# Kernel tuning notes

Measured on AMD Instinct MI355X. Metric: run time of the kernel, lower is better.

Reference implementation:

```python
import jax, jax.numpy as jnp
import numpy as np

N, E, D, H, FF = 50000, 1600000, 128, 8, 512
DK = D // H
EPS = 1e-5


def _layernorm(x, g, b):
    mu = jnp.mean(x, axis=-1, keepdims=True)
    var = jnp.mean((x - mu) ** 2, axis=-1, keepdims=True)
    return (x - mu) * jax.lax.rsqrt(var + EPS) * g + b


def setup_inputs() -> dict:
    key = jax.random.key(0)
    ks = jax.random.split(key, 10)
    s = 0.05
    return {
        "h": jax.random.normal(ks[0], (N, D), jnp.float32),
        "src": jax.random.randint(ks[1], (E,), 0, N, jnp.int32),
        "dst": jax.random.randint(ks[2], (E,), 0, N, jnp.int32),
        "Wq": jax.random.normal(ks[3], (D, D), jnp.float32) * s,
        "Wk": jax.random.normal(ks[4], (D, D), jnp.float32) * s,
        "Wv": jax.random.normal(ks[5], (D, D), jnp.float32) * s,
        "Wo": jax.random.normal(ks[6], (D, D), jnp.float32) * s,
        "ln1_g": jnp.ones((D,), jnp.float32),
        "ln1_b": jnp.zeros((D,), jnp.float32),
        "ln2_g": jnp.ones((D,), jnp.float32),
        "ln2_b": jnp.zeros((D,), jnp.float32),
        "W1": jax.random.normal(ks[7], (D, FF), jnp.float32) * s,
        "b1": jnp.zeros((FF,), jnp.float32),
        "W2": jax.random.normal(ks[8], (FF, D), jnp.float32) * s,
        "b2": jnp.zeros((D,), jnp.float32),
    }


def reference(h, src, dst, Wq, Wk, Wv, Wo, ln1_g, ln1_b, ln2_g, ln2_b, W1, b1, W2, b2):
    # QKV projections (bias-free, as in the torch module)
    q = (h @ Wq).reshape(N, H, DK)
    k = (h @ Wk).reshape(N, H, DK)
    v = (h @ Wv).reshape(N, H, DK)

    # masked_mm: per-edge, per-head score  e[m,h] = q[dst[m]] . k[src[m]]
    e = jnp.einsum("ehd,ehd->eh", q[dst], k[src]) / np.sqrt(DK)

    # sparse_softmax: segment softmax over incoming edges of each dst node
    m = jax.ops.segment_max(e, dst, num_segments=N)  # [N, H]
    ex = jnp.exp(e - m[dst])
    denom = jax.ops.segment_sum(ex, dst, num_segments=N)  # [N, H]
    alpha = ex / denom[dst]  # [E, H]

    # vec_spmm: a[n] = sum_{edges m with dst[m]==n} alpha[m] * v[src[m]]
    a = jax.ops.segment_sum(alpha[:, :, None] * v[src], dst, num_segments=N)
    a = a.reshape(N, D)

    o = a @ Wo
    h1 = _layernorm(h + o, ln1_g, ln1_b)
    ffn = jax.nn.relu(h1 @ W1 + b1) @ W2 + b2
    h2 = _layernorm(h1 + ffn, ln2_g, ln2_b)
    return h2
```

## Files before the change

kernel.cpp:

```cpp
#include <hip/hip_runtime.h>
#include <hip/hip_bf16.h>
#include <math.h>

#define D   128
#define FFD 512
#define NPART 8
#define BINB 1024
#define BCAP 768
#define NPROD 32
#define NSUB 32
#define RCAP 320

typedef __attribute__((ext_vector_type(8))) short bf16x8;
typedef __attribute__((ext_vector_type(4))) float f32x4;
typedef __attribute__((ext_vector_type(2))) float f32x2;

static inline size_t align256(size_t x){ return (x + 255) & ~(size_t)255; }

__device__ __forceinline__ float bf2f(unsigned short u){
    union { unsigned int i; float f; } x; x.i = ((unsigned int)u) << 16; return x.f;
}
__device__ __forceinline__ unsigned short f2bf(float f){
    return __builtin_bit_cast(unsigned short, __float2bfloat16(f));
}
__device__ __forceinline__ unsigned char f2fp8(float f){
    return (unsigned char)(__builtin_amdgcn_cvt_pk_fp8_f32(f, f, 0, false) & 0xff);
}

#define DPP_ADD(x, ctrl) do { \
    int yi_ = __builtin_amdgcn_update_dpp(0, __builtin_bit_cast(int, x), ctrl, 0xf, 0xf, true); \
    x += __builtin_bit_cast(float, yi_); } while(0)

__global__ __launch_bounds__(256) void k_bin3(const int* __restrict__ src,
                                              const int* __restrict__ dst, int E, int N,
                                              unsigned long long* __restrict__ pairs,
                                              int* __restrict__ lens,
                                              unsigned long long* __restrict__ spill,
                                              int* __restrict__ qspill){
    __shared__ int lcur[8];
    int tid = threadIdx.x;
    if (tid < 8) lcur[tid] = 0;
    __syncthreads();
    int slice = (N + 7) >> 3;
    int T = gridDim.x * 256;
    unsigned long long* myreg = pairs + (size_t)blockIdx.x * 8 * BCAP;
    for (int i = blockIdx.x*256 + tid; i < E; i += T){
        int d = __builtin_nontemporal_load(&dst[i]);
        int s = __builtin_nontemporal_load(&src[i]);
        int b = min(d / slice, 7);
        unsigned long long pr = ((unsigned long long)(unsigned)d << 32) | (unsigned)s;
        int slot = atomicAdd(&lcur[b], 1);
        if (slot < BCAP) myreg[(size_t)b*BCAP + slot] = pr;
        else { int p = atomicAdd(qspill, 1); spill[p] = pr; }
    }
    __syncthreads();
    if (tid < 8) lens[blockIdx.x*8 + tid] = min(lcur[tid], BCAP);
}

__global__ __launch_bounds__(256) void k_rebin(const unsigned long long* __restrict__ pairs,
                                               const int* __restrict__ lens,
                                               unsigned* __restrict__ pairs2,
                                               int* __restrict__ rlens,
                                               unsigned long long* __restrict__ spill,
                                               int* __restrict__ qspill, int N){
    __shared__ int lcur[NSUB];
    int part = blockIdx.x & 7, ip = blockIdx.x >> 3;
    int tid = threadIdx.x;
    if (tid < NSUB) lcur[tid] = 0;
    __syncthreads();
    int slice = (N + 7) >> 3;
    unsigned subslice = (unsigned)(slice + NSUB - 1) / NSUB;
    int lo_part = part * slice;
    unsigned* outbase = pairs2 + (size_t)(part*NPROD + ip) * NSUB * RCAP;
    for (int seg = ip*(BINB/NPROD); seg < (ip+1)*(BINB/NPROD); ++seg){
        int len = lens[seg*8 + part];
        const unsigned long long* pp = pairs + ((size_t)seg*8 + part)*BCAP;
        for (int i = tid; i < len; i += 256){
            unsigned long long pr = pp[i];
            int d = (int)(pr >> 32);
            unsigned dl = (unsigned)(d - lo_part);
            unsigned sb = dl / subslice;
            int slot = atomicAdd(&lcur[sb], 1);
            if (slot < RCAP)
                outbase[(size_t)sb*RCAP + slot] = ((dl - sb*subslice) << 24) | (unsigned)pr & 0xFFFFFFu;
            else { int p = atomicAdd(qspill, 1); spill[p] = pr; }
        }
    }
    __syncthreads();
    if (tid < NSUB) rlens[(part*NPROD + ip)*NSUB + tid] = min(lcur[tid], RCAP);
}

__global__ __launch_bounds__(256) void k_count4(const unsigned* __restrict__ pairs2,
                                                const int* __restrict__ rlens,
                                                const unsigned long long* __restrict__ spill,
                                                const int* __restrict__ qspill,
                                                int* __restrict__ cnt, int N){
    __shared__ int hist[256];
    int part = blockIdx.x & 7, s = blockIdx.x >> 3;
    int slice = (N + 7) >> 3;
    int subslice = (slice + NSUB - 1) / NSUB;
    int lo_part = part*slice;
    int lo = lo_part + s*subslice;
    int part_end = min(lo_part + slice, N);
    int n_sub = max(0, min(subslice, part_end - lo));
    for (int i = threadIdx.x; i < 256; i += 256) hist[i] = 0;
    __syncthreads();
    for (int ip = 0; ip < NPROD; ++ip){
        int r = (part*NPROD + ip)*NSUB + s;
        int len = rlens[r];
        const unsigned* pp = pairs2 + (size_t)r*RCAP;
        for (int i = threadIdx.x; i < len; i += 256)
            atomicAdd(&hist[pp[i] >> 24], 1);
    }
    int ns = *qspill;
    for (int i = threadIdx.x; i < ns; i += 256){
        int r = (int)(spill[i] >> 32) - lo;
        if (r >= 0 && r < n_sub) atomicAdd(&hist[r], 1);
    }
    __syncthreads();
    for (int i = threadIdx.x; i < n_sub; i += 256) cnt[lo + i] = hist[i];
}

__global__ __launch_bounds__(256) void k_scatter4(const unsigned* __restrict__ pairs2,
                                                  const int* __restrict__ rlens,
                                                  const unsigned long long* __restrict__ spill,
                                                  const int* __restrict__ qspill,
                                                  const int* __restrict__ off,
                                                  int* __restrict__ csr_src, int N){
    __shared__ int curl[256];
    int part = blockIdx.x & 7, s = blockIdx.x >> 3;
    int slice = (N + 7) >> 3;
    int subslice = (slice + NSUB - 1) / NSUB;
    int lo_part = part*slice;
    int lo = lo_part + s*subslice;
    int part_end = min(lo_part + slice, N);
    int n_sub = max(0, min(subslice, part_end - lo));
    for (int i = threadIdx.x; i < n_sub; i += 256) curl[i] = off[lo + i];
    __syncthreads();
    for (int ip = 0; ip < NPROD; ++ip){
        int r = (part*NPROD + ip)*NSUB + s;
        int len = rlens[r];
        const unsigned* pp = pairs2 + (size_t)r*RCAP;
        for (int i = threadIdx.x; i < len; i += 256){
            unsigned e = pp[i];
            int pos = atomicAdd(&curl[e >> 24], 1);
            csr_src[pos] = (int)(e & 0xFFFFFFu);
        }
    }
    int ns = *qspill;
    for (int i = threadIdx.x; i < ns; i += 256){
        unsigned long long pr = spill[i];
        int r = (int)(pr >> 32) - lo;
        if (r >= 0 && r < n_sub){
            int pos = atomicAdd(&curl[r], 1);
            csr_src[pos] = (int)(unsigned)pr;
        }
    }
}

__global__ __launch_bounds__(256) void k_bsum(const int* __restrict__ cnt, int N,
                                              int* __restrict__ bsum){
    int id = blockIdx.x*256 + threadIdx.x;
    int v = (id < N) ? cnt[id] : 0;
    #pragma unroll
    for (int o = 1; o < 64; o <<= 1) v += __shfl_xor(v, o);
    __shared__ int w4[4];
    if ((threadIdx.x & 63) == 0) w4[threadIdx.x >> 6] = v;
    __syncthreads();
    if (threadIdx.x == 0) bsum[blockIdx.x] = w4[0] + w4[1] + w4[2] + w4[3];
}

__global__ __launch_bounds__(1024) void k_scanb(const int* __restrict__ bsum, int NB,
                                                int* __restrict__ ebase,
                                                int* __restrict__ off, int N){
    __shared__ int sh[1024];
    int tid = threadIdx.x;
    int v = (tid < NB) ? bsum[tid] : 0;
    sh[tid] = v; __syncthreads();
    for (int o = 1; o < 1024; o <<= 1){
        int t = (tid >= o) ? sh[tid-o] : 0;
        __syncthreads();
        sh[tid] += t;
        __syncthreads();
    }
    if (tid < NB) ebase[tid] = sh[tid] - v;
    if (tid == NB-1) off[N] = sh[tid];
}

__global__ __launch_bounds__(256) void k_off(const int* __restrict__ cnt, int N,
                                             const int* __restrict__ ebase,
                                             int* __restrict__ off){
    __shared__ int sh[256];
    int tid = threadIdx.x;
    int id = blockIdx.x*256 + tid;
    int v = (id < N) ? cnt[id] : 0;
    sh[tid] = v; __syncthreads();
    for (int o = 1; o < 256; o <<= 1){
        int t = (tid >= o) ? sh[tid-o] : 0;
        __syncthreads();
        sh[tid] += t;
        __syncthreads();
    }
    int excl = sh[tid] - v;
    int base = ebase[blockIdx.x];
    if (id < N) off[id] = base + excl;
}

__global__ __launch_bounds__(256) void k_cast(const float* __restrict__ x,
                                              __hip_bfloat16* __restrict__ y, int n4){
    int i = blockIdx.x*blockDim.x + threadIdx.x;
    if (i >= n4) return;
    float4 f = ((const float4*)x)[i];
    ushort4 u;
    u.x = f2bf(f.x); u.y = f2bf(f.y);
    u.z = f2bf(f.z); u.w = f2bf(f.w);
    ((ushort4*)y)[i] = u;
}

__global__ __launch_bounds__(256) void k_prep_all(
    const float* __restrict__ Wq, const float* __restrict__ Wk,
    const float* __restrict__ Wv, const float* __restrict__ Wo,
    const float* __restrict__ W1, const float* __restrict__ W2,
    __hip_bfloat16* __restrict__ Wqkvt, __hip_bfloat16* __restrict__ Wot,
    __hip_bfloat16* __restrict__ W1t,   __hip_bfloat16* __restrict__ W2t){
    const float* W; __hip_bfloat16* Wt; int K, Nc;
    int y = blockIdx.y;
    switch (y){
        case 0: W = Wq; Wt = Wqkvt; K = 128; Nc = 128; break;
        case 1: W = Wk; Wt = Wqkvt; K = 128; Nc = 128; break;
        case 2: W = Wv; Wt = Wqkvt; K = 128; Nc = 128; break;
        case 3: W = Wo; Wt = Wot;   K = 128; Nc = 128; break;
        case 4: W = W1; Wt = W1t;   K = 128; Nc = 512; break;
        default: W = W2; Wt = W2t;  K = 512; Nc = 128; break;
    }
    int total = K*Nc;
    for (int id = blockIdx.x*256 + threadIdx.x; id < total; id += 256*gridDim.x){
        int n = id / K, kk = id % K;
        size_t drow;
        if (y == 1)      drow = 128 + 8*(n>>2) + (n&3);
        else if (y == 2) drow = 128 + 8*(n>>2) + 4 + (n&3);
        else             drow = n;
        Wt[drow*K + kk] = __float2bfloat16(W[(size_t)kk*Nc + n]);
    }
}

#define BM 128
#define BN 128
#define BK 64

__device__ __forceinline__ bool tile_coords(int M, int &r0, int &c0){
    int ncols = gridDim.x;
    int f = blockIdx.y * ncols + blockIdx.x;
    int xcd = f & 7, s = f >> 3;
    int c = s % ncols, rl = s / ncols;
    int r = rl*8 + xcd;
    r0 = r*BM; c0 = c*BN;
    return r0 < M;
}

__device__ __forceinline__ void stage_tile(const __hip_bfloat16* __restrict__ src,
                                           int row_base, int row_limit, int ldK, int k0,
                                           __hip_bfloat16* lds){
    int tid = threadIdx.x;
    int wave = tid >> 6;
    #pragma unroll
    for (int i = 0; i < 4; ++i){
        int c = i*256 + tid;
        int r = c >> 3, s = c & 7;
        int sg = s ^ (r & 7);
        int gr = row_base + r; if (gr >= row_limit) gr = row_limit - 1;
        const __hip_bfloat16* gp = src + (size_t)gr*ldK + k0 + sg*8;
        char* lp = (char*)lds + (i*256 + wave*64)*16;
        __builtin_amdgcn_global_load_lds((const __attribute__((address_space(1))) void*)gp,
                                         (__attribute__((address_space(3))) void*)lp,
                                         16, 0, 0);
    }
}

__device__ __forceinline__ bf16x8 frag(const __hip_bfloat16* buf, int R, int kk, int ls){
    int sl = (kk*4 + ls) ^ (R & 7);
    return *(const bf16x8*)((const char*)buf + R*128 + sl*16);
}

__global__ __launch_bounds__(256) void k_gemm_qkv(
    const __hip_bfloat16* __restrict__ A,
    const __hip_bfloat16* __restrict__ Bt,
    int M,
    __hip_bfloat16* __restrict__ qb, unsigned char* __restrict__ kvq){
    __shared__ __hip_bfloat16 As[BM*BK];
    __shared__ __hip_bfloat16 Bs[BN*BK];
    int r0, c0;
    if (!tile_coords(M, r0, c0)) return;
    int tid = threadIdx.x;
    int lane = tid & 63, wave = tid >> 6;
    int wr = wave >> 1, wc = wave & 1;
    int lr = lane & 15, ls = lane >> 4;

    f32x4 acc[4][4];
    #pragma unroll
    for (int m = 0; m < 4; m++)
        #pragma unroll
        for (int n = 0; n < 4; n++) acc[m][n] = (f32x4){0.f,0.f,0.f,0.f};

    for (int k0 = 0; k0 < 128; k0 += BK){
        stage_tile(A,  r0, M,   128, k0, As);
        stage_tile(Bt, c0, 384, 128, k0, Bs);
        __syncthreads();
        #pragma unroll
        for (int kk = 0; kk < 2; ++kk){
            bf16x8 af[4], bfg[4];
            #pragma unroll
            for (int m = 0; m < 4; m++) af[m]  = frag(As, wr*64 + m*16 + lr, kk, ls);
            #pragma unroll
            for (int n = 0; n < 4; n++) bfg[n] = frag(Bs, wc*64 + n*16 + lr, kk, ls);
            #pragma unroll
            for (int m = 0; m < 4; m++)
                #pragma unroll
                for (int n = 0; n < 4; n++)
                    acc[m][n] = __builtin_amdgcn_mfma_f32_16x16x32_bf16(af[m], bfg[n], acc[m][n], 0, 0, 0);
        }
        __syncthreads();
    }

    int region = c0 >> 7;
    #pragma unroll
    for (int n = 0; n < 4; n++){
        int c16 = wc*64 + n*16 + lr;
        #pragma unroll
        for (int m = 0; m < 4; m++){
            #pragma unroll
            for (int j = 0; j < 4; j++){
                int row = r0 + wr*64 + m*16 + ls*4 + j;
                if (row >= M) continue;
                float v = acc[m][n][j];
                if (region == 0)
                    ((unsigned short*)qb)[(size_t)row*128 + c16] = f2bf(v);
                else
                    kvq[(size_t)row*256 + (region-1)*128 + c16] = f2fp8(v);
            }
        }
    }
}

__global__ __launch_bounds__(256) void k_tail(
    const __hip_bfloat16* __restrict__ ab, const float* __restrict__ h,
    const __hip_bfloat16* __restrict__ Wot,
    const float* __restrict__ ln1g, const float* __restrict__ ln1b,
    const __hip_bfloat16* __restrict__ W1t, const float* __restrict__ b1,
    const __hip_bfloat16* __restrict__ W2t, const float* __restrict__ b2,
    const float* __restrict__ ln2g, const float* __restrict__ ln2b,
    float* __restrict__ out, int M){
    __shared__ __hip_bfloat16 As[BM*BK];
    __shared__ __hip_bfloat16 Bs[BM*BK];
    __shared__ __hip_bfloat16 h1s[2][BM*BK];
    __shared__ __hip_bfloat16 t1s[2][BM*BK];
    __shared__ float red[2][BM][2];
    int f = blockIdx.x;
    int r0 = ((f >> 3)*8 + (f & 7)) * BM;
    if (r0 >= M) return;
    int tid = threadIdx.x;
    int lane = tid & 63, wave = tid >> 6;
    int wr = wave >> 1, wc = wave & 1;
    int lr = lane & 15, ls = lane >> 4;

    f32x4 acc[4][4];
    #pragma unroll
    for (int m = 0; m < 4; m++)
        #pragma unroll
        for (int n = 0; n < 4; n++) acc[m][n] = (f32x4){0.f,0.f,0.f,0.f};

    for (int k0 = 0; k0 < 128; k0 += BK){
        stage_tile(ab,  r0, M,   128, k0, As);
        stage_tile(Wot, 0,  128, 128, k0, Bs);
        __syncthreads();
        #pragma unroll
        for (int kk = 0; kk < 2; ++kk){
            bf16x8 af[4], bfg[4];
            #pragma unroll
            for (int m = 0; m < 4; m++) af[m]  = frag(As, wr*64 + m*16 + lr, kk, ls);
            #pragma unroll
            for (int n = 0; n < 4; n++) bfg[n] = frag(Bs, wc*64 + n*16 + lr, kk, ls);
            #pragma unroll
            for (int m = 0; m < 4; m++)
                #pragma unroll
                for (int n = 0; n < 4; n++)
                    acc[m][n] = __builtin_amdgcn_mfma_f32_16x16x32_bf16(af[m], bfg[n], acc[m][n], 0, 0, 0);
        }
        __syncthreads();
    }

    #pragma unroll
    for (int m = 0; m < 4; m++){
        #pragma unroll
        for (int j = 0; j < 4; j++){
            int rowl = wr*64 + m*16 + ls*4 + j;
            int row = r0 + rowl;
            float s = 0.f, q = 0.f;
            #pragma unroll
            for (int n = 0; n < 4; n++){
                int col = wc*64 + n*16 + lr;
                float rv = (row < M) ? h[(size_t)row*128 + col] : 0.f;
                float v = acc[m][n][j] + rv;
                acc[m][n][j] = v;
                s += v; q += v*v;
            }
            #pragma unroll
            for (int o = 1; o < 16; o <<= 1){
                s += __shfl_xor(s, o);
                q += __shfl_xor(q, o);
            }
            if (lr == 0){
                red[0][rowl][wc] = s;
                red[1][rowl][wc] = q;
            }
        }
    }
    __syncthreads();
    #pragma unroll
    for (int m = 0; m < 4; m++){
        #pragma unroll
        for (int j = 0; j < 4; j++){
            int rowl = wr*64 + m*16 + ls*4 + j;
            float mu  = (red[0][rowl][0] + red[0][rowl][1]) * (1.f/128.f);
            float eq  = (red[1][rowl][0] + red[1][rowl][1]) * (1.f/128.f);
            float var = fmaxf(eq - mu*mu, 0.f);
            float inv = rsqrtf(var + 1e-5f);
            #pragma unroll
            for (int n = 0; n < 4; n++){
                int col = wc*64 + n*16 + lr;
                float o = (acc[m][n][j] - mu)*inv*ln1g[col] + ln1b[col];
                int half = col >> 6, c6 = col & 63;
                int slot = (c6 >> 3) ^ (rowl & 7), elem = c6 & 7;
                ((unsigned short*)h1s[half])[rowl*64 + slot*8 + elem] = f2bf(o);
            }
        }
    }
    __syncthreads();

    f32x4 yacc[4][4];
    #pragma unroll
    for (int m = 0; m < 4; m++)
        #pragma unroll
        for (int n = 0; n < 4; n++) yacc[m][n] = (f32x4){0.f,0.f,0.f,0.f};

    for (int c = 0; c < 4; ++c){
        f32x4 tacc[4][4];
        #pragma unroll
        for (int m = 0; m < 4; m++)
            #pragma unroll
            for (int n = 0; n < 4; n++) tacc[m][n] = (f32x4){0.f,0.f,0.f,0.f};
        for (int step = 0; step < 2; ++step){
            stage_tile(W1t, c*128, 512, 128, step*64, Bs);
            __syncthreads();
            #pragma unroll
            for (int kk = 0; kk < 2; ++kk){
                bf16x8 af[4], bfg[4];
                #pragma unroll
                for (int m = 0; m < 4; m++) af[m]  = frag(h1s[step], wr*64 + m*16 + lr, kk, ls);
                #pragma unroll
                for (int n = 0; n < 4; n++) bfg[n] = frag(Bs, wc*64 + n*16 + lr, kk, ls);
                #pragma unroll
                for (int m = 0; m < 4; m++)
                    #pragma unroll
                    for (int n = 0; n < 4; n++)
                        tacc[m][n] = __builtin_amdgcn_mfma_f32_16x16x32_bf16(af[m], bfg[n], tacc[m][n], 0, 0, 0);
            }
            __syncthreads();
        }
        #pragma unroll
        for (int m = 0; m < 4; m++){
            #pragma unroll
            for (int j = 0; j < 4; j++){
                int rowl = wr*64 + m*16 + ls*4 + j;
                #pragma unroll
                for (int n = 0; n < 4; n++){
                    int col = wc*64 + n*16 + lr;
                    float v = fmaxf(tacc[m][n][j] + b1[c*128 + col], 0.f);
                    int half = col >> 6, c6 = col & 63;
                    int slot = (c6 >> 3) ^ (rowl & 7), elem = c6 & 7;
                    ((unsigned short*)t1s[half])[rowl*64 + slot*8 + elem] = f2bf(v);
                }
            }
        }
        __syncthreads();
        for (int step = 0; step < 2; ++step){
            stage_tile(W2t, 0, 128, 512, c*128 + step*64, Bs);
            __syncthreads();
            #pragma unroll
            for (int kk = 0; kk < 2; ++kk){
                bf16x8 af[4], bfg[4];
                #pragma unroll
                for (int m = 0; m < 4; m++) af[m]  = frag(t1s[step], wr*64 + m*16 + lr, kk, ls);
                #pragma unroll
                for (int n = 0; n < 4; n++) bfg[n] = frag(Bs, wc*64 + n*16 + lr, kk, ls);
                #pragma unroll
                for (int m = 0; m < 4; m++)
                    #pragma unroll
                    for (int n = 0; n < 4; n++)
                        yacc[m][n] = __builtin_amdgcn_mfma_f32_16x16x32_bf16(af[m], bfg[n], yacc[m][n], 0, 0, 0);
            }
            __syncthreads();
        }
    }

    #pragma unroll
    for (int m = 0; m < 4; m++){
        #pragma unroll
        for (int j = 0; j < 4; j++){
            int rowl = wr*64 + m*16 + ls*4 + j;
            float s = 0.f, q = 0.f;
            #pragma unroll
            for (int n = 0; n < 4; n++){
                int col = wc*64 + n*16 + lr;
                int half = col >> 6, c6 = col & 63;
                int slot = (c6 >> 3) ^ (rowl & 7), elem = c6 & 7;
                float h1v = bf2f(((const unsigned short*)h1s[half])[rowl*64 + slot*8 + elem]);
                float v = yacc[m][n][j] + b2[col] + h1v;
                yacc[m][n][j] = v;
                s += v; q += v*v;
            }
            #pragma unroll
            for (int o = 1; o < 16; o <<= 1){
                s += __shfl_xor(s, o);
                q += __shfl_xor(q, o);
            }
            if (lr == 0){
                red[0][rowl][wc] = s;
                red[1][rowl][wc] = q;
            }
        }
    }
    __syncthreads();
    #pragma unroll
    for (int m = 0; m < 4; m++){
        #pragma unroll
        for (int j = 0; j < 4; j++){
            int rowl = wr*64 + m*16 + ls*4 + j;
            int row = r0 + rowl;
            if (row >= M) continue;
            float mu  = (red[0][rowl][0] + red[0][rowl][1]) * (1.f/128.f);
            float eq  = (red[1][rowl][0] + red[1][rowl][1]) * (1.f/128.f);
            float var = fmaxf(eq - mu*mu, 0.f);
            float inv = rsqrtf(var + 1e-5f);
            #pragma unroll
            for (int n = 0; n < 4; n++){
                int col = wc*64 + n*16 + lr;
                out[(size_t)row*128 + col] = (yacc[m][n][j] - mu)*inv*ln2g[col] + ln2b[col];
            }
        }
    }
}

#define PAIR(jj, dd, b0, b1, b2, b3) { \
    int s0_ = __builtin_amdgcn_readlane(myidx, (jj)); \
    int s1_ = __builtin_amdgcn_readlane(myidx, (jj)+1); \
    int sv_ = half ? s1_ : s0_; \
    uint2 u_ = kv[(size_t)(unsigned)sv_*32 + l32]; \
    f32x2 k01 = __builtin_amdgcn_cvt_pk_f32_fp8((int)u_.x, false); \
    f32x2 k23 = __builtin_amdgcn_cvt_pk_f32_fp8((int)u_.x, true); \
    f32x2 v01 = __builtin_amdgcn_cvt_pk_f32_fp8((int)u_.y, false); \
    f32x2 v23 = __builtin_amdgcn_cvt_pk_f32_fp8((int)u_.y, true); \
    float p_ = q0*k01[0] + q1*k01[1] + q2*k23[0] + q3*k23[1]; \
    DPP_ADD(p_, 0xB1); DPP_ADD(p_, 0x4E); \
    float w_ = __builtin_amdgcn_exp2f(p_); \
    dd += w_; \
    b0 = fmaf(w_, v01[0], b0); b1 = fmaf(w_, v01[1], b1); \
    b2 = fmaf(w_, v23[0], b2); b3 = fmaf(w_, v23[1], b3); }

#define PAIRV(jj, dd, b0, b1, b2, b3) { \
    int s0_ = __builtin_amdgcn_readlane(myidx, (jj)); \
    int s1_ = __builtin_amdgcn_readlane(myidx, min((jj)+1, 63)); \
    int sv_ = half ? s1_ : s0_; \
    uint2 u_ = kv[(size_t)(unsigned)sv_*32 + l32]; \
    f32x2 k01 = __builtin_amdgcn_cvt_pk_f32_fp8((int)u_.x, false); \
    f32x2 k23 = __builtin_amdgcn_cvt_pk_f32_fp8((int)u_.x, true); \
    f32x2 v01 = __builtin_amdgcn_cvt_pk_f32_fp8((int)u_.y, false); \
    f32x2 v23 = __builtin_amdgcn_cvt_pk_f32_fp8((int)u_.y, true); \
    float p_ = q0*k01[0] + q1*k01[1] + q2*k23[0] + q3*k23[1]; \
    DPP_ADD(p_, 0xB1); DPP_ADD(p_, 0x4E); \
    float w_ = __builtin_amdgcn_exp2f(p_); \
    if ((jj) + half >= cnt) w_ = 0.f; \
    dd += w_; \
    b0 = fmaf(w_, v01[0], b0); b1 = fmaf(w_, v01[1], b1); \
    b2 = fmaf(w_, v23[0], b2); b3 = fmaf(w_, v23[1], b3); }

__global__ __launch_bounds__(256) void k_attn(const __hip_bfloat16* __restrict__ qb,
                                              const uint2* __restrict__ kv,
                                              const int* __restrict__ off,
                                              const int* __restrict__ csr_src,
                                              __hip_bfloat16* __restrict__ a, int N){
    int wid = (blockIdx.x*blockDim.x + threadIdx.x) >> 6;
    int lane = threadIdx.x & 63;
    if (wid >= N) return;
    int half = lane >> 5, l32 = lane & 31;
    ushort4 qu = ((const ushort4*)(qb + (size_t)wid*128))[l32];
    const float SC = 0.25f * 1.44269504f;
    float q0 = bf2f(qu.x)*SC, q1 = bf2f(qu.y)*SC, q2 = bf2f(qu.z)*SC, q3 = bf2f(qu.w)*SC;
    int beg = off[wid], end = off[wid+1];
    float dA=0, a0A=0, a1A=0, a2A=0, a3A=0;
    float dB=0, a0B=0, a1B=0, a2B=0, a3B=0;
    for (int e0 = beg; e0 < end; e0 += 64){
        int myidx = (e0 + lane < end) ? csr_src[e0 + lane] : 0;
        int cnt = min(64, end - e0);
        int j = 0;
        for (; j + 3 < cnt; j += 4){
            PAIR(j,   dA, a0A, a1A, a2A, a3A);
            PAIR(j+2, dB, a0B, a1B, a2B, a3B);
        }
        for (; j < cnt; j += 2){
            PAIRV(j, dA, a0A, a1A, a2A, a3A);
        }
    }
    float d  = dA + dB;
    float a0 = a0A + a0B, a1 = a1A + a1B, a2 = a2A + a2B, a3 = a3A + a3B;
    d  += __shfl_xor(d, 32);
    a0 += __shfl_xor(a0, 32);
    a1 += __shfl_xor(a1, 32);
    a2 += __shfl_xor(a2, 32);
    a3 += __shfl_xor(a3, 32);
    if (half == 0){
        float r = (d > 0.f) ? 1.f/d : 0.f;
        ushort4 o;
        o.x = f2bf(a0*r); o.y = f2bf(a1*r); o.z = f2bf(a2*r); o.w = f2bf(a3*r);
        ((ushort4*)(a + (size_t)wid*128))[l32] = o;
    }
}

extern "C" void kernel_launch(void* const* d_in, const int* in_sizes, int n_in,
                              void* d_out, int out_size, void* d_ws, size_t ws_size,
                              hipStream_t stream){
    const float* h    = (const float*)d_in[0];
    const int*   src  = (const int*)  d_in[1];
    const int*   dst  = (const int*)  d_in[2];
    const float* Wq   = (const float*)d_in[3];
    const float* Wk   = (const float*)d_in[4];
    const float* Wv   = (const float*)d_in[5];
    const float* Wo   = (const float*)d_in[6];
    const float* ln1g = (const float*)d_in[7];
    const float* ln1b = (const float*)d_in[8];
    const float* ln2g = (const float*)d_in[9];
    const float* ln2b = (const float*)d_in[10];
    const float* W1   = (const float*)d_in[11];
    const float* b1   = (const float*)d_in[12];
    const float* W2   = (const float*)d_in[13];
    const float* b2   = (const float*)d_in[14];
    float* out = (float*)d_out;

    const int N = in_sizes[0] / D;
    const int E = in_sizes[1];

    char* ws = (char*)d_ws;
    size_t o = 0;
    const size_t row_bf = align256((size_t)N * D * sizeof(__hip_bfloat16));
    const size_t kv_q   = align256((size_t)N * 256);

    __hip_bfloat16* qb  = (__hip_bfloat16*)(ws + o); o += row_bf;
    unsigned char* kvq  = (unsigned char*)(ws + o); o += kv_q;
    __hip_bfloat16* ab  = (__hip_bfloat16*)(ws + o); o += row_bf;
    __hip_bfloat16* hb  = (__hip_bfloat16*)(ws + o); o += row_bf;
    __hip_bfloat16* Wqkvt = (__hip_bfloat16*)(ws + o); o += align256(384*128*2);
    __hip_bfloat16* W1t   = (__hip_bfloat16*)(ws + o); o += align256(512*128*2);
    __hip_bfloat16* W2t   = (__hip_bfloat16*)(ws + o); o += align256(128*512*2);
    __hip_bfloat16* Wot   = (__hip_bfloat16*)(ws + o); o += align256(128*128*2);
    int* cnt   = (int*)(ws + o); o += align256((size_t)N*4);
    int* offp  = (int*)(ws + o); o += align256((size_t)(N+1)*4);
    int* bsum  = (int*)(ws + o); o += align256(1024*4);
    int* ebase = (int*)(ws + o); o += align256(1024*4);
    int* lens  = (int*)(ws + o); o += align256((size_t)BINB*8*4);
    int* rlens = (int*)(ws + o); o += align256((size_t)NPART*NPROD*NSUB*4);
    int* qspill= (int*)(ws + o); o += align256(256);
    int* csr   = (int*)(ws + o); o += align256((size_t)E*4);
    unsigned long long* pairs = (unsigned long long*)(ws + o);
    o += align256((size_t)BINB * 8 * BCAP * 8);
    unsigned* pairs2 = (unsigned*)(ws + o);
    o += align256((size_t)NPART * NPROD * NSUB * RCAP * 4);
    unsigned long long* spill = (unsigned long long*)(ws + o);
    o += align256((size_t)E * 8);

    const int NB = (N + 255)/256;

    (void)hipMemsetAsync(qspill, 0, 256, stream);
    k_bin3<<<BINB, 256, 0, stream>>>(src, dst, E, N, pairs, lens, spill, qspill);

    k_cast<<<(N*D/4 + 255)/256, 256, 0, stream>>>(h, hb, N*D/4);
    k_prep_all<<<dim3(64, 6), 256, 0, stream>>>(Wq, Wk, Wv, Wo, W1, W2,
                                                Wqkvt, Wot, W1t, W2t);

    k_rebin<<<NPART*NPROD, 256, 0, stream>>>(pairs, lens, pairs2, rlens, spill, qspill, N);
    k_count4<<<NPART*NSUB, 256, 0, stream>>>(pairs2, rlens, spill, qspill, cnt, N);
    k_bsum <<<NB, 256, 0, stream>>>(cnt, N, bsum);
    k_scanb<<<1, 1024, 0, stream>>>(bsum, NB, ebase, offp, N);
    k_off  <<<NB, 256, 0, stream>>>(cnt, N, ebase, offp);
    k_scatter4<<<NPART*NSUB, 256, 0, stream>>>(pairs2, rlens, spill, qspill, offp, csr, N);

    int mb = (N + BM - 1)/BM;
    int mb_pad = ((mb + 7)/8)*8;

    k_gemm_qkv<<<dim3(3, mb_pad), 256, 0, stream>>>(hb, Wqkvt, N, qb, kvq);

    k_attn<<<(N*64 + 255)/256, 256, 0, stream>>>(qb, (const uint2*)kvq, offp, csr, ab, N);

    k_tail<<<mb_pad, 256, 0, stream>>>(ab, h, Wot, ln1g, ln1b,
                                       W1t, b1, W2t, b2, ln2g, ln2b, out, N);
}
```

Before: 230.5 us.

## Shrink FFN chunk to 64 columns in fused tail kernel to cut LDS

The fused tail kernel now walks the FFN hidden dimension in eight chunks of 64 instead of four chunks of 128. Each chunk stages the whole 64x128 W1 slice at once, and the activation tile reuses one 16KB buffer instead of a dedicated 32KB t1s array. This cuts LDS per block by about a third and removes several barriers, which should allow more resident blocks per CU. In exchange each chunk launches fewer MFMAs per barrier, the W2 tile is staged more often, and tacc uses fewer registers.

```diff
diff --git a/kernel.cpp b/kernel.cpp
--- a/kernel.cpp
+++ b/kernel.cpp
@@ -277,6 +277,24 @@
     }
 }
 
+__device__ __forceinline__ void stage_rows64(const __hip_bfloat16* __restrict__ src,
+                                             int row_base, int ldK, int k0,
+                                             __hip_bfloat16* lds){
+    int tid = threadIdx.x;
+    int wave = tid >> 6;
+    #pragma unroll
+    for (int i = 0; i < 2; ++i){
+        int c = i*256 + tid;
+        int r = c >> 3, s = c & 7;
+        int sg = s ^ (r & 7);
+        const __hip_bfloat16* gp = src + (size_t)(row_base + r)*ldK + k0 + sg*8;
+        char* lp = (char*)lds + (i*256 + wave*64)*16;
+        __builtin_amdgcn_global_load_lds((const __attribute__((address_space(1))) void*)gp,
+                                         (__attribute__((address_space(3))) void*)lp,
+                                         16, 0, 0);
+    }
+}
+
 __device__ __forceinline__ bf16x8 frag(const __hip_bfloat16* buf, int R, int kk, int ls){
     int sl = (kk*4 + ls) ^ (R & 7);
     return *(const bf16x8*)((const char*)buf + R*128 + sl*16);
@@ -350,10 +368,9 @@
     const __hip_bfloat16* __restrict__ W2t, const float* __restrict__ b2,
     const float* __restrict__ ln2g, const float* __restrict__ ln2b,
     float* __restrict__ out, int M){
-    __shared__ __hip_bfloat16 As[BM*BK];
-    __shared__ __hip_bfloat16 Bs[BM*BK];
+    __shared__ __hip_bfloat16 buf0[BM*BK];
+    __shared__ __hip_bfloat16 buf1[BM*BK];
     __shared__ __hip_bfloat16 h1s[2][BM*BK];
-    __shared__ __hip_bfloat16 t1s[2][BM*BK];
     __shared__ float red[2][BM][2];
     int f = blockIdx.x;
     int r0 = ((f >> 3)*8 + (f & 7)) * BM;
@@ -370,16 +387,16 @@
         for (int n = 0; n < 4; n++) acc[m][n] = (f32x4){0.f,0.f,0.f,0.f};
 
     for (int k0 = 0; k0 < 128; k0 += BK){
-        stage_tile(ab,  r0, M,   128, k0, As);
-        stage_tile(Wot, 0,  128, 128, k0, Bs);
+        stage_tile(ab,  r0, M,   128, k0, buf0);
+        stage_tile(Wot, 0,  128, 128, k0, buf1);
         __syncthreads();
         #pragma unroll
         for (int kk = 0; kk < 2; ++kk){
             bf16x8 af[4], bfg[4];
             #pragma unroll
-            for (int m = 0; m < 4; m++) af[m]  = frag(As, wr*64 + m*16 + lr, kk, ls);
-            #pragma unroll
-            for (int n = 0; n < 4; n++) bfg[n] = frag(Bs, wc*64 + n*16 + lr, kk, ls);
+            for (int m = 0; m < 4; m++) af[m]  = frag(buf0, wr*64 + m*16 + lr, kk, ls);
+            #pragma unroll
+            for (int n = 0; n < 4; n++) bfg[n] = frag(buf1, wc*64 + n*16 + lr, kk, ls);
             #pragma unroll
             for (int m = 0; m < 4; m++)
                 #pragma unroll
@@ -429,9 +446,9 @@
             for (int n = 0; n < 4; n++){
                 int col = wc*64 + n*16 + lr;
                 float o = (acc[m][n][j] - mu)*inv*ln1g[col] + ln1b[col];
-                int half = col >> 6, c6 = col & 63;
+                int hh = col >> 6, c6 = col & 63;
                 int slot = (c6 >> 3) ^ (rowl & 7), elem = c6 & 7;
-                ((unsigned short*)h1s[half])[rowl*64 + slot*8 + elem] = f2bf(o);
+                ((unsigned short*)h1s[hh])[rowl*64 + slot*8 + elem] = f2bf(o);
             }
         }
     }
@@ -443,29 +460,30 @@
         #pragma unroll
         for (int n = 0; n < 4; n++) yacc[m][n] = (f32x4){0.f,0.f,0.f,0.f};
 
-    for (int c = 0; c < 4; ++c){
-        f32x4 tacc[4][4];
+    for (int c = 0; c < 8; ++c){
+        stage_rows64(W1t, c*64, 128, 0,  buf1);
+        stage_rows64(W1t, c*64, 128, 64, buf1 + 64*64);
+        __syncthreads();
+        f32x4 tacc[4][2];
         #pragma unroll
         for (int m = 0; m < 4; m++)
             #pragma unroll
-            for (int n = 0; n < 4; n++) tacc[m][n] = (f32x4){0.f,0.f,0.f,0.f};
+            for (int n = 0; n < 2; n++) tacc[m][n] = (f32x4){0.f,0.f,0.f,0.f};
+        #pragma unroll
         for (int step = 0; step < 2; ++step){
-            stage_tile(W1t, c*128, 512, 128, step*64, Bs);
-            __syncthreads();
             #pragma unroll
             for (int kk = 0; kk < 2; ++kk){
-                bf16x8 af[4], bfg[4];
+                bf16x8 af[4], bfg[2];
                 #pragma unroll
                 for (int m = 0; m < 4; m++) af[m]  = frag(h1s[step], wr*64 + m*16 + lr, kk, ls);
                 #pragma unroll
-                for (int n = 0; n < 4; n++) bfg[n] = frag(Bs, wc*64 + n*16 + lr, kk, ls);
+                for (int n = 0; n < 2; n++) bfg[n] = frag(buf1 + step*64*64, wc*32 + n*16 + lr, kk, ls);
                 #pragma unroll
                 for (int m = 0; m < 4; m++)
                     #pragma unroll
-                    for (int n = 0; n < 4; n++)
+                    for (int n = 0; n < 2; n++)
                         tacc[m][n] = __builtin_amdgcn_mfma_f32_16x16x32_bf16(af[m], bfg[n], tacc[m][n], 0, 0, 0);
             }
-            __syncthreads();
         }
         #pragma unroll
         for (int m = 0; m < 4; m++){
@@ -473,34 +491,31 @@
             for (int j = 0; j < 4; j++){
                 int rowl = wr*64 + m*16 + ls*4 + j;
                 #pragma unroll
-                for (int n = 0; n < 4; n++){
-                    int col = wc*64 + n*16 + lr;
-                    float v = fmaxf(tacc[m][n][j] + b1[c*128 + col], 0.f);
-                    int half = col >> 6, c6 = col & 63;
-                    int slot = (c6 >> 3) ^ (rowl & 7), elem = c6 & 7;
-                    ((unsigned short*)t1s[half])[rowl*64 + slot*8 + elem] = f2bf(v);
+                for (int n = 0; n < 2; n++){
+                    int cc = wc*32 + n*16 + lr;
+                    float v = fmaxf(tacc[m][n][j] + b1[c*64 + cc], 0.f);
+                    int slot = (cc >> 3) ^ (rowl & 7), elem = cc & 7;
+                    ((unsigned short*)buf0)[rowl*64 + slot*8 + elem] = f2bf(v);
                 }
             }
         }
         __syncthreads();
-        for (int step = 0; step < 2; ++step){
-            stage_tile(W2t, 0, 128, 512, c*128 + step*64, Bs);
-            __syncthreads();
-            #pragma unroll
-            for (int kk = 0; kk < 2; ++kk){
-                bf16x8 af[4], bfg[4];
+        stage_tile(W2t, 0, 128, 512, c*64, buf1);
+        __syncthreads();
+        #pragma unroll
+        for (int kk = 0; kk < 2; ++kk){
+            bf16x8 af[4], bfg[4];
+            #pragma unroll
+            for (int m = 0; m < 4; m++) af[m]  = frag(buf0, wr*64 + m*16 + lr, kk, ls);
+            #pragma unroll
+            for (int n = 0; n < 4; n++) bfg[n] = frag(buf1, wc*64 + n*16 + lr, kk, ls);
+            #pragma unroll
+            for (int m = 0; m < 4; m++)
                 #pragma unroll
-                for (int m = 0; m < 4; m++) af[m]  = frag(t1s[step], wr*64 + m*16 + lr, kk, ls);
-                #pragma unroll
-                for (int n = 0; n < 4; n++) bfg[n] = frag(Bs, wc*64 + n*16 + lr, kk, ls);
-                #pragma unroll
-                for (int m = 0; m < 4; m++)
-                    #pragma unroll
-                    for (int n = 0; n < 4; n++)
-                        yacc[m][n] = __builtin_amdgcn_mfma_f32_16x16x32_bf16(af[m], bfg[n], yacc[m][n], 0, 0, 0);
-            }
-            __syncthreads();
-        }
+                for (int n = 0; n < 4; n++)
+                    yacc[m][n] = __builtin_amdgcn_mfma_f32_16x16x32_bf16(af[m], bfg[n], yacc[m][n], 0, 0, 0);
+        }
+        __syncthreads();
     }
 
     #pragma unroll
@@ -512,9 +527,9 @@
             #pragma unroll
             for (int n = 0; n < 4; n++){
                 int col = wc*64 + n*16 + lr;
-                int half = col >> 6, c6 = col & 63;
+                int hh = col >> 6, c6 = col & 63;
                 int slot = (c6 >> 3) ^ (rowl & 7), elem = c6 & 7;
-                float h1v = bf2f(((const unsigned short*)h1s[half])[rowl*64 + slot*8 + elem]);
+                float h1v = bf2f(((const unsigned short*)h1s[hh])[rowl*64 + slot*8 + elem]);
                 float v = yacc[m][n][j] + b2[col] + h1v;
                 yacc[m][n][j] = v;
                 s += v; q += v*v;
```

New measurement: 235.3 us. +2.1%, slower.
